# Kernel optimization log

Measured on AMD Instinct MI355X. Metric: run time of the kernel, lower is better.

The kernel has to match this reference:

```python
import jax, jax.numpy as jnp
import numpy as np

B, S, H = 16, 4096, 1024


def setup_inputs() -> dict:
    key = jax.random.key(0)
    ks = jax.random.split(key, 8)
    scale = 1.0 / np.sqrt(H)
    return {
        "s_t_hat": jax.random.normal(ks[0], (B, H), jnp.float32),
        "encoder_outputs": jax.random.normal(ks[1], (B, S, H), jnp.float32),
        "encoder_feature": jax.random.normal(ks[2], (B * S, H), jnp.float32),
        "enc_padding_mask": jnp.ones((B, S), jnp.float32),
        "coverage": jax.random.uniform(ks[3], (B, S), jnp.float32),
        # params: decode_proj (Linear H->H with bias), W_c (Linear 1->H, no bias,
        # stored as an [H] column), v (Linear H->1, no bias, stored as [H])
        "W_dec": jax.random.normal(ks[4], (H, H), jnp.float32) * scale,
        "b_dec": jnp.zeros((H,), jnp.float32),
        "W_c": jax.random.normal(ks[5], (H,), jnp.float32),
        "v": jax.random.normal(ks[6], (H,), jnp.float32) * scale,
    }


def reference(s_t_hat, encoder_outputs, encoder_feature, enc_padding_mask,
              coverage, W_dec, b_dec, W_c, v):
    b, s, h = encoder_outputs.shape
    # decode_proj: [B, H]
    dec_fea = s_t_hat @ W_dec.T + b_dec
    # broadcast add over seq + coverage feature (Linear(1->H) == outer product)
    att = (encoder_feature.reshape(b, s, h)
           + dec_fea[:, None, :]
           + coverage[:, :, None] * W_c[None, None, :])
    e = jnp.tanh(att)
    scores = jnp.einsum('bsh,h->bs', e, v)
    # masked softmax with renormalization (is_word=True path)
    attn = jax.nn.softmax(scores, axis=1) * enc_padding_mask
    attn = attn / (attn.sum(axis=1, keepdims=True) + 1e-20)
    # context vector: weighted sum of encoder outputs
    c_t = jnp.einsum('bs,bsh->bh', attn, encoder_outputs)
    return c_t, attn, attn, scores
```

## Files before the change

kernel.cpp:

```cpp
#include <hip/hip_runtime.h>

#define BB 16
#define SS 4096
#define HH 1024
#define SSPLIT 64

__device__ __forceinline__ float fast_tanh(float x) {
    x = fminf(fmaxf(x, -15.0f), 15.0f);
    float e = __expf(-2.0f * x);
    return (1.0f - e) * __builtin_amdgcn_rcpf(1.0f + e);
}

__device__ __forceinline__ float wave_reduce_sum(float v) {
#pragma unroll
    for (int off = 32; off > 0; off >>= 1) v += __shfl_xor(v, off, 64);
    return v;
}

__global__ __launch_bounds__(256) void dec_fea_kernel(
    const float* __restrict__ s_t_hat, const float* __restrict__ W_dec,
    const float* __restrict__ b_dec, float* __restrict__ dec_fea)
{
    int wave = (blockIdx.x * blockDim.x + threadIdx.x) >> 6;
    int lane = threadIdx.x & 63;
    int b = wave >> 10;
    int h = wave & (HH - 1);
    const float4* st4 = (const float4*)(s_t_hat + (size_t)b * HH);
    const float4* wd4 = (const float4*)(W_dec + (size_t)h * HH);
    float acc = 0.0f;
#pragma unroll
    for (int j = 0; j < 4; ++j) {
        int idx = lane + 64 * j;
        float4 a = st4[idx];
        float4 w = wd4[idx];
        acc += a.x * w.x + a.y * w.y + a.z * w.z + a.w * w.w;
    }
    acc = wave_reduce_sum(acc);
    if (lane == 0) dec_fea[wave] = acc + b_dec[h];
}

__global__ __launch_bounds__(256) void scores_kernel(
    const float* __restrict__ ef, const float* __restrict__ dec_fea,
    const float* __restrict__ cov, const float* __restrict__ W_c,
    const float* __restrict__ v, float* __restrict__ scores)
{
    int row = (blockIdx.x * blockDim.x + threadIdx.x) >> 6;
    int lane = threadIdx.x & 63;
    int b = row >> 12;
    float cv = cov[row];
    const float4* ef4 = (const float4*)(ef + (size_t)row * HH);
    const float4* de4 = (const float4*)(dec_fea + (size_t)b * HH);
    const float4* wc4 = (const float4*)W_c;
    const float4* v4  = (const float4*)v;
    float acc = 0.0f;
#pragma unroll
    for (int j = 0; j < 4; ++j) {
        int idx = lane + 64 * j;
        float4 x  = ef4[idx];
        float4 d  = de4[idx];
        float4 w  = wc4[idx];
        float4 vv = v4[idx];
        acc += fast_tanh(x.x + d.x + cv * w.x) * vv.x;
        acc += fast_tanh(x.y + d.y + cv * w.y) * vv.y;
        acc += fast_tanh(x.z + d.z + cv * w.z) * vv.z;
        acc += fast_tanh(x.w + d.w + cv * w.w) * vv.w;
    }
    acc = wave_reduce_sum(acc);
    if (lane == 0) scores[row] = acc;
}

__global__ __launch_bounds__(1024) void softmax_kernel(
    const float* __restrict__ scores, const float* __restrict__ mask,
    float* __restrict__ attn1, float* __restrict__ attn2)
{
    int b = blockIdx.x;
    int tid = threadIdx.x;

    const float4* s4 = (const float4*)(scores + (size_t)b * SS);
    const float4* m4 = (const float4*)(mask + (size_t)b * SS);
    float4 sc = s4[tid];
    float4 mk = m4[tid];

    __shared__ float redA[16];
    __shared__ float redB[16];
    int wid = tid >> 6, lane = tid & 63;

    float mx = fmaxf(fmaxf(sc.x, sc.y), fmaxf(sc.z, sc.w));
#pragma unroll
    for (int off = 32; off > 0; off >>= 1) mx = fmaxf(mx, __shfl_xor(mx, off, 64));
    if (lane == 0) redA[wid] = mx;
    __syncthreads();
    float bm = redA[0];
#pragma unroll
    for (int i = 1; i < 16; ++i) bm = fmaxf(bm, redA[i]);
    __syncthreads();

    float4 e;
    e.x = __expf(sc.x - bm);
    e.y = __expf(sc.y - bm);
    e.z = __expf(sc.z - bm);
    e.w = __expf(sc.w - bm);
    float4 t;
    t.x = e.x * mk.x; t.y = e.y * mk.y; t.z = e.z * mk.z; t.w = e.w * mk.w;

    float se = wave_reduce_sum(e.x + e.y + e.z + e.w);
    float st = wave_reduce_sum(t.x + t.y + t.z + t.w);
    if (lane == 0) { redA[wid] = se; redB[wid] = st; }
    __syncthreads();
    float tot_e = 0.0f, tot_t = 0.0f;
#pragma unroll
    for (int i = 0; i < 16; ++i) { tot_e += redA[i]; tot_t += redB[i]; }

    float inv = 1.0f / tot_e;
    float r = 1.0f / (tot_t * inv + 1e-20f);
    float scale = inv * r;
    float4 a;
    a.x = t.x * scale; a.y = t.y * scale; a.z = t.z * scale; a.w = t.w * scale;
    ((float4*)(attn1 + (size_t)b * SS))[tid] = a;
    ((float4*)(attn2 + (size_t)b * SS))[tid] = a;
}

__global__ __launch_bounds__(256) void context_partial_kernel(
    const float* __restrict__ eo, const float* __restrict__ attn,
    float* __restrict__ partials)
{
    int b = blockIdx.y;
    int s0 = blockIdx.x * (SS / SSPLIT);
    int tid = threadIdx.x;
    const float4* eo4 = (const float4*)(eo + ((size_t)b * SS + s0) * HH);
    const float* at = attn + (size_t)b * SS + s0;
    float4 acc = {0.0f, 0.0f, 0.0f, 0.0f};
#pragma unroll 8
    for (int s = 0; s < SS / SSPLIT; ++s) {
        float a = at[s];
        float4 x = eo4[(size_t)s * 256 + tid];
        acc.x += a * x.x; acc.y += a * x.y; acc.z += a * x.z; acc.w += a * x.w;
    }
    float4* dst = (float4*)(partials + ((size_t)blockIdx.x * BB + b) * HH);
    dst[tid] = acc;
}

__global__ __launch_bounds__(256) void context_reduce_kernel(
    const float* __restrict__ partials, float* __restrict__ c_t)
{
    int gid = blockIdx.x * blockDim.x + threadIdx.x;
    const float4* p4 = (const float4*)partials;
    float4 acc = {0.0f, 0.0f, 0.0f, 0.0f};
#pragma unroll
    for (int s = 0; s < SSPLIT; ++s) {
        float4 x = p4[(size_t)s * (BB * HH / 4) + gid];
        acc.x += x.x; acc.y += x.y; acc.z += x.z; acc.w += x.w;
    }
    ((float4*)c_t)[gid] = acc;
}

extern "C" void kernel_launch(void* const* d_in, const int* in_sizes, int n_in,
                              void* d_out, int out_size, void* d_ws, size_t ws_size,
                              hipStream_t stream)
{
    const float* s_t_hat  = (const float*)d_in[0];
    const float* enc_out  = (const float*)d_in[1];
    const float* enc_feat = (const float*)d_in[2];
    const float* mask     = (const float*)d_in[3];
    const float* cov      = (const float*)d_in[4];
    const float* W_dec    = (const float*)d_in[5];
    const float* b_dec    = (const float*)d_in[6];
    const float* W_c      = (const float*)d_in[7];
    const float* v        = (const float*)d_in[8];

    float* out    = (float*)d_out;
    float* c_t    = out;
    float* attn1  = out + BB * HH;
    float* attn2  = attn1 + BB * SS;
    float* scores = attn2 + BB * SS;

    float* dec_fea  = (float*)d_ws;
    float* partials = dec_fea + BB * HH;

    dec_fea_kernel<<<dim3(BB * HH / 4), 256, 0, stream>>>(s_t_hat, W_dec, b_dec, dec_fea);
    scores_kernel<<<dim3(BB * SS / 4), 256, 0, stream>>>(enc_feat, dec_fea, cov, W_c, v, scores);
    softmax_kernel<<<dim3(BB), 1024, 0, stream>>>(scores, mask, attn1, attn2);
    context_partial_kernel<<<dim3(SSPLIT, BB), 256, 0, stream>>>(enc_out, attn1, partials);
    context_reduce_kernel<<<dim3(BB * HH / 1024), 256, 0, stream>>>(partials, c_t);
}
```

Before: 522.9 us.

## Fuse softmax into scores kernel with atomics and defer normalization to finalize

Computes exp(score) and masked exp directly in the scores kernel, accumulating per-batch sums via atomics, eliminating the separate softmax kernel. The context reduction uses unnormalized weights and a final kernel applies the normalization scale to both attn outputs and c_t. Split count for the context partials is doubled for more parallelism. Drops max-subtraction, risking overflow for large scores, and adds atomic contention.

```diff
diff --git a/kernel.cpp b/kernel.cpp
--- a/kernel.cpp
+++ b/kernel.cpp
@@ -3,7 +3,8 @@
 #define BB 16
 #define SS 4096
 #define HH 1024
-#define SSPLIT 64
+#define SPLIT 128
+#define CHUNK (SS / SPLIT)
 
 __device__ __forceinline__ float fast_tanh(float x) {
     x = fminf(fmaxf(x, -15.0f), 15.0f);
@@ -19,8 +20,10 @@
 
 __global__ __launch_bounds__(256) void dec_fea_kernel(
     const float* __restrict__ s_t_hat, const float* __restrict__ W_dec,
-    const float* __restrict__ b_dec, float* __restrict__ dec_fea)
+    const float* __restrict__ b_dec, float* __restrict__ dec_fea,
+    float* __restrict__ stats)
 {
+    if (blockIdx.x == 0) stats[threadIdx.x] = 0.0f;
     int wave = (blockIdx.x * blockDim.x + threadIdx.x) >> 6;
     int lane = threadIdx.x & 63;
     int b = wave >> 10;
@@ -42,10 +45,13 @@
 __global__ __launch_bounds__(256) void scores_kernel(
     const float* __restrict__ ef, const float* __restrict__ dec_fea,
     const float* __restrict__ cov, const float* __restrict__ W_c,
-    const float* __restrict__ v, float* __restrict__ scores)
+    const float* __restrict__ v, const float* __restrict__ mask,
+    float* __restrict__ scores, float* __restrict__ tbuf,
+    float* __restrict__ stats)
 {
     int row = (blockIdx.x * blockDim.x + threadIdx.x) >> 6;
     int lane = threadIdx.x & 63;
+    int wid = threadIdx.x >> 6;
     int b = row >> 12;
     float cv = cov[row];
     const float4* ef4 = (const float4*)(ef + (size_t)row * HH);
@@ -66,92 +72,77 @@
         acc += fast_tanh(x.w + d.w + cv * w.w) * vv.w;
     }
     acc = wave_reduce_sum(acc);
-    if (lane == 0) scores[row] = acc;
-}
 
-__global__ __launch_bounds__(1024) void softmax_kernel(
-    const float* __restrict__ scores, const float* __restrict__ mask,
-    float* __restrict__ attn1, float* __restrict__ attn2)
-{
-    int b = blockIdx.x;
-    int tid = threadIdx.x;
-
-    const float4* s4 = (const float4*)(scores + (size_t)b * SS);
-    const float4* m4 = (const float4*)(mask + (size_t)b * SS);
-    float4 sc = s4[tid];
-    float4 mk = m4[tid];
-
-    __shared__ float redA[16];
-    __shared__ float redB[16];
-    int wid = tid >> 6, lane = tid & 63;
-
-    float mx = fmaxf(fmaxf(sc.x, sc.y), fmaxf(sc.z, sc.w));
-#pragma unroll
-    for (int off = 32; off > 0; off >>= 1) mx = fmaxf(mx, __shfl_xor(mx, off, 64));
-    if (lane == 0) redA[wid] = mx;
+    __shared__ float sh_e[4];
+    __shared__ float sh_t[4];
+    if (lane == 0) {
+        scores[row] = acc;
+        float e = __expf(acc);
+        float t = e * mask[row];
+        tbuf[row] = t;
+        sh_e[wid] = e;
+        sh_t[wid] = t;
+    }
     __syncthreads();
-    float bm = redA[0];
-#pragma unroll
-    for (int i = 1; i < 16; ++i) bm = fmaxf(bm, redA[i]);
-    __syncthreads();
-
-    float4 e;
-    e.x = __expf(sc.x - bm);
-    e.y = __expf(sc.y - bm);
-    e.z = __expf(sc.z - bm);
-    e.w = __expf(sc.w - bm);
-    float4 t;
-    t.x = e.x * mk.x; t.y = e.y * mk.y; t.z = e.z * mk.z; t.w = e.w * mk.w;
-
-    float se = wave_reduce_sum(e.x + e.y + e.z + e.w);
-    float st = wave_reduce_sum(t.x + t.y + t.z + t.w);
-    if (lane == 0) { redA[wid] = se; redB[wid] = st; }
-    __syncthreads();
-    float tot_e = 0.0f, tot_t = 0.0f;
-#pragma unroll
-    for (int i = 0; i < 16; ++i) { tot_e += redA[i]; tot_t += redB[i]; }
-
-    float inv = 1.0f / tot_e;
-    float r = 1.0f / (tot_t * inv + 1e-20f);
-    float scale = inv * r;
-    float4 a;
-    a.x = t.x * scale; a.y = t.y * scale; a.z = t.z * scale; a.w = t.w * scale;
-    ((float4*)(attn1 + (size_t)b * SS))[tid] = a;
-    ((float4*)(attn2 + (size_t)b * SS))[tid] = a;
+    if (threadIdx.x == 0) {
+        atomicAdd(&stats[b * 16 + 0], sh_e[0] + sh_e[1] + sh_e[2] + sh_e[3]);
+        atomicAdd(&stats[b * 16 + 1], sh_t[0] + sh_t[1] + sh_t[2] + sh_t[3]);
+    }
 }
 
 __global__ __launch_bounds__(256) void context_partial_kernel(
-    const float* __restrict__ eo, const float* __restrict__ attn,
+    const float* __restrict__ eo, const float* __restrict__ tbuf,
     float* __restrict__ partials)
 {
     int b = blockIdx.y;
-    int s0 = blockIdx.x * (SS / SSPLIT);
+    int s0 = blockIdx.x * CHUNK;
     int tid = threadIdx.x;
     const float4* eo4 = (const float4*)(eo + ((size_t)b * SS + s0) * HH);
-    const float* at = attn + (size_t)b * SS + s0;
+    const float* tt = tbuf + (size_t)b * SS + s0;
     float4 acc = {0.0f, 0.0f, 0.0f, 0.0f};
 #pragma unroll 8
-    for (int s = 0; s < SS / SSPLIT; ++s) {
-        float a = at[s];
-        float4 x = eo4[(size_t)s * 256 + tid];
+    for (int s = 0; s < CHUNK; ++s) {
+        float a = tt[s];
+        float4 x = eo4[(size_t)s * (HH / 4) + tid];
         acc.x += a * x.x; acc.y += a * x.y; acc.z += a * x.z; acc.w += a * x.w;
     }
     float4* dst = (float4*)(partials + ((size_t)blockIdx.x * BB + b) * HH);
     dst[tid] = acc;
 }
 
-__global__ __launch_bounds__(256) void context_reduce_kernel(
-    const float* __restrict__ partials, float* __restrict__ c_t)
+__global__ __launch_bounds__(256) void finalize_kernel(
+    const float* __restrict__ tbuf, const float* __restrict__ partials,
+    const float* __restrict__ stats, float* __restrict__ attn1,
+    float* __restrict__ attn2, float* __restrict__ c_t)
 {
-    int gid = blockIdx.x * blockDim.x + threadIdx.x;
-    const float4* p4 = (const float4*)partials;
-    float4 acc = {0.0f, 0.0f, 0.0f, 0.0f};
-#pragma unroll
-    for (int s = 0; s < SSPLIT; ++s) {
-        float4 x = p4[(size_t)s * (BB * HH / 4) + gid];
-        acc.x += x.x; acc.y += x.y; acc.z += x.z; acc.w += x.w;
+    int tid = threadIdx.x;
+    if (blockIdx.x < 64) {
+        int g = blockIdx.x * 256 + tid;
+        int b = g >> 10;
+        float se = stats[b * 16 + 0];
+        float st = stats[b * 16 + 1];
+        float scale = 1.0f / (st + 1e-20f * se);
+        float4 t = ((const float4*)tbuf)[g];
+        float4 a;
+        a.x = t.x * scale; a.y = t.y * scale; a.z = t.z * scale; a.w = t.w * scale;
+        ((float4*)attn1)[g] = a;
+        ((float4*)attn2)[g] = a;
+    } else {
+        int ci = (blockIdx.x - 64) * 256 + tid;
+        int b = ci >> 8;
+        float se = stats[b * 16 + 0];
+        float st = stats[b * 16 + 1];
+        float scale = 1.0f / (st + 1e-20f * se);
+        const float4* p4 = (const float4*)partials;
+        float4 acc = {0.0f, 0.0f, 0.0f, 0.0f};
+#pragma unroll 8
+        for (int s = 0; s < SPLIT; ++s) {
+            float4 x = p4[(size_t)s * (BB * HH / 4) + ci];
+            acc.x += x.x; acc.y += x.y; acc.z += x.z; acc.w += x.w;
+        }
+        acc.x *= scale; acc.y *= scale; acc.z *= scale; acc.w *= scale;
+        ((float4*)c_t)[ci] = acc;
     }
-    ((float4*)c_t)[gid] = acc;
 }
 
 extern "C" void kernel_launch(void* const* d_in, const int* in_sizes, int n_in,
@@ -175,11 +166,13 @@
     float* scores = attn2 + BB * SS;
 
     float* dec_fea  = (float*)d_ws;
-    float* partials = dec_fea + BB * HH;
+    float* tbuf     = dec_fea + BB * HH;
+    float* stats    = tbuf + BB * SS;
+    float* partials = stats + 256;
 
-    dec_fea_kernel<<<dim3(BB * HH / 4), 256, 0, stream>>>(s_t_hat, W_dec, b_dec, dec_fea);
-    scores_kernel<<<dim3(BB * SS / 4), 256, 0, stream>>>(enc_feat, dec_fea, cov, W_c, v, scores);
-    softmax_kernel<<<dim3(BB), 1024, 0, stream>>>(scores, mask, attn1, attn2);
-    context_partial_kernel<<<dim3(SSPLIT, BB), 256, 0, stream>>>(enc_out, attn1, partials);
-    context_reduce_kernel<<<dim3(BB * HH / 1024), 256, 0, stream>>>(partials, c_t);
+    dec_fea_kernel<<<dim3(BB * HH / 4), 256, 0, stream>>>(s_t_hat, W_dec, b_dec, dec_fea, stats);
+    scores_kernel<<<dim3(BB * SS / 4), 256, 0, stream>>>(enc_feat, dec_fea, cov, W_c, v, mask,
+                                                         scores, tbuf, stats);
+    context_partial_kernel<<<dim3(SPLIT, BB), 256, 0, stream>>>(enc_out, tbuf, partials);
+    finalize_kernel<<<dim3(80), 256, 0, stream>>>(tbuf, partials, stats, attn1, attn2, c_t);
 }
```

Result: slower. 597.4 us (+14.2%).
